# Kernel tuning notes

Measured on AMD Instinct MI355X. Metric: run time of the kernel, lower is better.

Reference implementation:

```python
import jax, jax.numpy as jnp
import numpy as np

BIG = 1e9  # finite stand-in for float('inf') so gradients stay clean
K_ITERS = 256  # Bellman-Ford relaxation sweeps (converges for paths up to K edges)
DIRS = [(-1, -1), (-1, 0), (-1, 1), (0, -1), (0, 1), (1, -1), (1, 0), (1, 1)]


def setup_inputs() -> dict:
    key = jax.random.key(0)
    ks = jax.random.split(key, 4)
    H, W, C = 256, 256, 128
    features = jax.random.normal(ks[0], (H, W, C), dtype=jnp.float32)
    return {
        "features": features,
        "delta": jnp.float32(0.1),
        "gamma": jnp.float32(1.0),
        "beta": jnp.float32(1.0),
        "w1": jax.random.normal(ks[1], (C, C // 4), dtype=jnp.float32) * 0.05,
        "b1": jnp.zeros((C // 4,), dtype=jnp.float32),
        "w2": jax.random.normal(ks[2], (C // 4, 1), dtype=jnp.float32) * 0.05,
        "b2": jnp.zeros((1,), dtype=jnp.float32),
        "start_node": jnp.zeros((2,), dtype=jnp.int32),
        "end_node": jnp.array([H - 1, W - 1], dtype=jnp.int32),
    }


def _avg_pool3(x):
    # x: (C, H, W); 3x3 avg pool, stride 1, pad 1, count_include_pad=True (torch default)
    s = jax.lax.reduce_window(x, 0.0, jax.lax.add, (1, 3, 3), (1, 1, 1),
                              ((0, 0), (1, 1), (1, 1)))
    return s / 9.0


def _heuristic_grid(features, delta, gamma, beta, w1, b1, w2, b2, end_node):
    H, W, C = features.shape
    all_feats = features.reshape(H * W, C)
    C_lf = C // 2
    feats_lf = all_feats[:, :C_lf]
    feats_hf = all_feats[:, C_lf:]

    # Sobel gradient magnitude per channel -> geodesic grid
    sobel_x = jnp.array([[-1, 0, 1], [-2, 0, 2], [-1, 0, 1]], dtype=features.dtype)
    sobel_y = jnp.array([[-1, -2, -1], [0, 0, 0], [1, 2, 1]], dtype=features.dtype)
    sobel = jnp.stack([sobel_x, sobel_y])[:, None]  # (2,1,3,3) OIHW
    x = jnp.transpose(features, (2, 0, 1))[:, None]  # (C,1,H,W)
    grad = jax.lax.conv_general_dilated(x, sobel, (1, 1), ((1, 1), (1, 1)),
                                        dimension_numbers=("NCHW", "OIHW", "NCHW"))
    grad_mag = jnp.sqrt(jnp.sum(grad * grad, axis=1))  # (C,H,W)
    geodesic_grid = jnp.mean(grad_mag, axis=0)  # (H,W)

    # Local variance of high-frequency channels
    hf = jnp.transpose(feats_hf.reshape(H, W, -1), (2, 0, 1))  # (C_hf,H,W)
    var_hf = jnp.sum(_avg_pool3(hf * hf) - _avg_pool3(hf) ** 2, axis=0)  # (H,W)
    info_goal_hf = var_hf[end_node[0], end_node[1]]
    scattering = info_goal_hf - var_hf

    # Absorption cost: distance of low-freq feats to goal low-freq feats
    end_feat_lf = feats_lf.reshape(H, W, -1)[end_node[0], end_node[1]]
    absorption = jnp.linalg.norm(feats_lf - end_feat_lf[None, :], axis=1).reshape(H, W)

    # Gating MLP
    h = jax.nn.relu(all_feats @ w1 + b1)
    omega = jax.nn.sigmoid(h @ w2 + b2).reshape(H, W)

    d, g, b = jax.nn.softplus(delta), jax.nn.softplus(gamma), jax.nn.softplus(beta)
    return jax.nn.relu(d * geodesic_grid + omega * g * scattering + (1 - omega) * b * absorption)


def _cost_grid(features):
    H, W, _ = features.shape
    fn = features / jnp.maximum(jnp.linalg.norm(features, axis=-1, keepdims=True), 1e-12)
    cost = jnp.full((H, W, 8), BIG, dtype=features.dtype)
    for i, (dx, dy) in enumerate(DIRS):
        sc_h = slice(max(0, -dx), H - max(0, dx))
        sc_w = slice(max(0, -dy), W - max(0, dy))
        sn_h = slice(max(0, dx), H + min(0, dx))
        sn_w = slice(max(0, dy), W + min(0, dy))
        sim = jnp.sum(fn[sc_h, sc_w] * fn[sn_h, sn_w], axis=-1)
        cost = cost.at[sc_h, sc_w, i].set(1.0 - sim)
    return cost


def _shift_big(a, dx, dy):
    H, W = a.shape
    p = jnp.pad(a, 1, constant_values=BIG)
    return jax.lax.dynamic_slice(p, (1 - dx, 1 - dy), (H, W))


def _distance_map(cost, start_node):
    # Parallel Bellman-Ford relaxation: equals the A* g_score map for shortest
    # paths with <= K_ITERS edges (nonnegative affinity costs).
    H, W, _ = cost.shape
    dist0 = jnp.full((H, W), BIG, dtype=cost.dtype).at[start_node[0], start_node[1]].set(0.0)

    def body(dist, _):
        d = dist
        for i, (dx, dy) in enumerate(DIRS):
            d = jnp.minimum(d, _shift_big(dist + cost[:, :, i], dx, dy))
        return d, None

    dist, _ = jax.lax.scan(body, dist0, None, length=K_ITERS)
    return jnp.minimum(dist, BIG)


def reference(features, delta, gamma, beta, w1, b1, w2, b2, start_node, end_node):
    heuristic = _heuristic_grid(features, delta, gamma, beta, w1, b1, w2, b2, end_node)
    cost = _cost_grid(features)
    dist = _distance_map(cost, start_node)
    # (H, W, 10): [heuristic | 8 directional edge costs | g_score distance map]
    return jnp.concatenate([heuristic[..., None], cost, dist[..., None]], axis=-1)
```

## Files before the change

### kernel.cpp

```cpp
#include <hip/hip_runtime.h>
#include <math.h>

#define Hd 256
#define Wd 256
#define Cd 128
#define BIGV 1.0e9f

static __device__ __forceinline__ float softplus_f(float x) {
    return fmaxf(x, 0.0f) + log1pf(expf(-fabsf(x)));
}

#define FMAXBITS 0x7F7FFFFF
template<int CTRL, int RM>
static __device__ __forceinline__ float dpp_mv(float x) {
    return __int_as_float(__builtin_amdgcn_update_dpp(
        FMAXBITS, __float_as_int(x), CTRL, RM, 0xF, false));
}
template<int CTRL, int RM>
static __device__ __forceinline__ float dpp_min(float x) {
    return fminf(x, dpp_mv<CTRL, RM>(x));
}
static __device__ __forceinline__ float wave_prefmin(float x) {
    x = dpp_min<0x111, 0xF>(x);
    x = dpp_min<0x112, 0xF>(x);
    x = dpp_min<0x114, 0xF>(x);
    x = dpp_min<0x118, 0xF>(x);
    x = dpp_min<0x142, 0xA>(x);
    x = dpp_min<0x143, 0xC>(x);
    return x;
}

#define TILE 16
#define HPX 18
#define PXN 324
#define SP  325
#define CHUNK 32

__global__ __launch_bounds__(256) void k_cost(
    const float* __restrict__ feat,
    float* __restrict__ out, float* __restrict__ costP)
{
    __shared__ float stage[CHUNK * SP];
    __shared__ float normL[PXN];

    const int t  = threadIdx.x;
    const int r0 = blockIdx.y * TILE;
    const int c0 = blockIdx.x * TILE;

    const int lr = t >> 4, lc = t & 15;
    const int r = r0 + lr, c = c0 + lc;
    const int px0 = (lr + 1) * HPX + (lc + 1);

    float dotv[8];
#pragma unroll
    for (int j = 0; j < 8; ++j) dotv[j] = 0.0f;

    for (int ch0 = 0; ch0 < Cd; ch0 += CHUNK) {
        __syncthreads();
        for (int i = t; i < PXN * 8; i += 256) {
            int px = i >> 3, f4 = i & 7;
            int pr = px / HPX;
            int pc = px - pr * HPX;
            int gr = r0 - 1 + pr, gc = c0 - 1 + pc;
            float4 v = make_float4(0.f, 0.f, 0.f, 0.f);
            if ((unsigned)gr < Hd && (unsigned)gc < Wd) {
                v = *reinterpret_cast<const float4*>(
                        &feat[(((gr << 8) + gc) * Cd) + ch0 + (f4 << 2)]);
            }
            int chb = f4 << 2;
            stage[(chb + 0) * SP + px] = v.x;
            stage[(chb + 1) * SP + px] = v.y;
            stage[(chb + 2) * SP + px] = v.z;
            stage[(chb + 3) * SP + px] = v.w;
        }
        __syncthreads();
        for (int px = t; px < PXN; px += 256) {
            float s = 0.0f;
#pragma unroll
            for (int ch = 0; ch < CHUNK; ++ch) {
                float v = stage[ch * SP + px];
                s = fmaf(v, v, s);
            }
            if (ch0 == 0) normL[px] = s; else normL[px] += s;
        }
        for (int ch = 0; ch < CHUNK; ++ch) {
            const float* pl = stage + ch * SP + px0;
            float x  = pl[0];
            float n0 = pl[-HPX - 1], n1 = pl[-HPX], n2 = pl[-HPX + 1];
            float n3 = pl[-1],                      n4 = pl[1];
            float n5 = pl[HPX - 1],  n6 = pl[HPX],  n7 = pl[HPX + 1];

            dotv[0] = fmaf(x, n0, dotv[0]);
            dotv[1] = fmaf(x, n1, dotv[1]);
            dotv[2] = fmaf(x, n2, dotv[2]);
            dotv[3] = fmaf(x, n3, dotv[3]);
            dotv[4] = fmaf(x, n4, dotv[4]);
            dotv[5] = fmaf(x, n5, dotv[5]);
            dotv[6] = fmaf(x, n6, dotv[6]);
            dotv[7] = fmaf(x, n7, dotv[7]);
        }
    }
    __syncthreads();

    const int p = (r << 8) + c;
    float np = fmaxf(sqrtf(normL[px0]), 1e-12f);
    const int drr[8] = {-1,-1,-1, 0, 0, 1, 1, 1};
    const int dcc[8] = {-1, 0, 1,-1, 1,-1, 0, 1};
    const int nof[8] = {-HPX-1,-HPX,-HPX+1,-1,1,HPX-1,HPX,HPX+1};
#pragma unroll
    for (int j = 0; j < 8; ++j) {
        int nr = r + drr[j], nc = c + dcc[j];
        float cj;
        if ((unsigned)nr < Hd && (unsigned)nc < Wd) {
            float nn = fmaxf(sqrtf(normL[px0 + nof[j]]), 1e-12f);
            cj = 1.0f - dotv[j] / (np * nn);
        } else {
            cj = BIGV;
        }
        costP[(j << 16) + p] = cj;
        out[p * 10 + 1 + j]  = cj;
    }
}

__global__ __launch_bounds__(64) void k_scan(
    const float* __restrict__ costP, float* __restrict__ PR, float* __restrict__ PRm)
{
    const int r = blockIdx.x;
    const int l = threadIdx.x;
    const int base = (r << 8) + (l << 2);

    {
        const float4 c4 = *(const float4*)&costP[(4 << 16) + base];
        float a0 = c4.x, a1 = a0 + c4.y, a2 = a1 + c4.z, a3 = a2 + c4.w;
        float ta = a3;
#pragma unroll
        for (int o = 1; o < 64; o <<= 1) {
            float xa = __shfl_up(ta, o, 64);
            if (l >= o) ta += xa;
        }
        float ea = __shfl_up(ta, 1, 64); if (l == 0) ea = 0.0f;
        float4 P; P.x = ea; P.y = ea + a0; P.z = ea + a1; P.w = ea + a2;
        *(float4*)&PR[base] = P;
    }
    {
        const float4 m = *(const float4*)&costP[(3 << 16) + (r << 8) + (252 - (l << 2))];
        float w0 = m.w, w1_ = m.z, w2_ = m.y, w3 = m.x;
        float a0 = w0, a1 = a0 + w1_, a2 = a1 + w2_, a3 = a2 + w3;
        float ta = a3;
#pragma unroll
        for (int o = 1; o < 64; o <<= 1) {
            float xa = __shfl_up(ta, o, 64);
            if (l >= o) ta += xa;
        }
        float ea = __shfl_up(ta, 1, 64); if (l == 0) ea = 0.0f;
        float4 P; P.x = ea; P.y = ea + a0; P.z = ea + a1; P.w = ea + a2;
        *(float4*)&PRm[base] = P;
    }
}

#define PIPE 8

static __device__ __forceinline__ float4 ld4m(const float* p, int r, int l, int M) {
    if (!M) return *(const float4*)&p[(r << 8) + (l << 2)];
    float4 v = *(const float4*)&p[(r << 8) + (252 - (l << 2))];
    return make_float4(v.w, v.z, v.y, v.x);
}

__global__ __launch_bounds__(256) void k_main(
    const float* __restrict__ feat,
    const float* __restrict__ w1, const float* __restrict__ b1,
    const float* __restrict__ w2, const float* __restrict__ b2,
    const float* __restrict__ dlt, const float* __restrict__ gmm,
    const float* __restrict__ bta, const int* __restrict__ endn,
    const float* __restrict__ costP, const float* __restrict__ PR,
    const float* __restrict__ PRm, const int* __restrict__ startn,
    float* __restrict__ out, float* __restrict__ distQ)
{
    if (blockIdx.x < 4) {
        const int l = threadIdx.x;
        if (l >= 64) return;
        const int sw = blockIdx.x;
        const int M     = sw & 1;
        const int vdown = (sw < 2);
        const int sr = startn[0];
        const int sc = M ? (255 - startn[1]) : startn[1];
        const float* __restrict__ PRu = M ? PRm : PR;
        const int pInc = vdown ? (M ? 5 : 7) : (M ? 0 : 2);
        const int pStr = vdown ? 6 : 1;
        const int pDec = vdown ? (M ? 7 : 5) : (M ? 2 : 0);
        const float* __restrict__ cInP = costP + (pInc << 16);
        const float* __restrict__ cStP = costP + (pStr << 16);
        const float* __restrict__ cDeP = costP + (pDec << 16);
        float* __restrict__ O = distQ + (sw << 16);
        const int iStart = vdown ? sr : (255 - sr);

        const float4 BIG4 = make_float4(BIGV, BIGV, BIGV, BIGV);

        float4 sv = BIG4;
        {
            int kk = sc - (l << 2);
            if (kk == 0) sv.x = 0.0f;
            if (kk == 1) sv.y = 0.0f;
            if (kk == 2) sv.z = 0.0f;
            if (kk == 3) sv.w = 0.0f;
        }

#define ROW_OF(ii)  (vdown ? ((ii) > 255 ? 255 : (ii)) : (255 - ((ii) > 255 ? 255 : (ii))))
#define ROWP_OF(ii) (vdown ? (((ii) - 1) < 0 ? 0 : (((ii) - 1) > 255 ? 255 : ((ii) - 1))) \
                           : (255 - (((ii) - 1) < 0 ? 0 : (((ii) - 1) > 255 ? 255 : ((ii) - 1)))))

        float4 bPR[PIPE], bI[PIPE], bS[PIPE], bD[PIPE];
#pragma unroll
        for (int k = 0; k < PIPE; ++k) {
            int rP = ROW_OF(k), rC = ROWP_OF(k);
            bPR[k] = *(const float4*)&PRu[(rP << 8) + (l << 2)];
            bI[k]  = ld4m(cInP, rC, l, M);
            bS[k]  = ld4m(cStP, rC, l, M);
            bD[k]  = ld4m(cDeP, rC, l, M);
        }

        float4 Dp = BIG4;
        for (int ib = 0; ib < 256; ib += PIPE) {
#pragma unroll
            for (int k = 0; k < PIPE; ++k) {
                const int i = ib + k;
                const int r = vdown ? i : 255 - i;
                float4 PR_c = bPR[k], cI_c = bI[k], cS_c = bS[k], cD_c = bD[k];

                float tS0 = Dp.x + cS_c.x, tS1 = Dp.y + cS_c.y,
                      tS2 = Dp.z + cS_c.z, tS3 = Dp.w + cS_c.w;
                float tI0 = Dp.x + cI_c.x, tI1 = Dp.y + cI_c.y,
                      tI2 = Dp.z + cI_c.z, tI3 = Dp.w + cI_c.w;
                float tD0 = Dp.x + cD_c.x, tD1 = Dp.y + cD_c.y,
                      tD2 = Dp.z + cD_c.z, tD3 = Dp.w + cD_c.w;
                float tIm = dpp_mv<0x138, 0xF>(tI3);
                float tDn = dpp_mv<0x130, 0xF>(tD0);
                float4 cand;
                cand.x = fminf(tS0, fminf(tIm, tD1));
                cand.y = fminf(tS1, fminf(tI0, tD2));
                cand.z = fminf(tS2, fminf(tI1, tD3));
                cand.w = fminf(tS3, fminf(tI2, tDn));
                if (i == iStart) {
                    cand.x = fminf(cand.x, sv.x);
                    cand.y = fminf(cand.y, sv.y);
                    cand.z = fminf(cand.z, sv.z);
                    cand.w = fminf(cand.w, sv.w);
                }
                float z0 = cand.x - PR_c.x;
                float z1 = fminf(cand.y - PR_c.y, z0);
                float z2 = fminf(cand.z - PR_c.z, z1);
                float z3 = fminf(cand.w - PR_c.w, z2);
                float w  = wave_prefmin(z3);
                float e  = dpp_mv<0x138, 0xF>(w);
                float4 D;
                D.x = PR_c.x + fminf(z0, e);
                D.y = PR_c.y + fminf(z1, e);
                D.z = PR_c.z + fminf(z2, e);
                D.w = PR_c.w + fminf(z3, e);

                *(float4*)&O[(r << 8) + (l << 2)] = D;
                Dp = D;

                {
                    const int jn = i + PIPE;
                    int rP = ROW_OF(jn), rC = ROWP_OF(jn);
                    bPR[k] = *(const float4*)&PRu[(rP << 8) + (l << 2)];
                    bI[k]  = ld4m(cInP, rC, l, M);
                    bS[k]  = ld4m(cStP, rC, l, M);
                    bD[k]  = ld4m(cDeP, rC, l, M);
                }
            }
        }
#undef ROW_OF
#undef ROWP_OF
        return;
    }

    __shared__ float  stage[CHUNK * SP];
    __shared__ float4 w1L[Cd * 8];
    __shared__ float  endfL[64];
    __shared__ float  vendL[64];
    __shared__ float  vendS;

    const int t  = threadIdx.x;
    const int b  = blockIdx.x - 4;
    const int r0 = (b >> 4) * TILE;
    const int c0 = (b & 15) * TILE;

    for (int i = t; i < Cd * 8; i += 256) w1L[i] = ((const float4*)w1)[i];
    const int er = endn[0], ec = endn[1];
    if (t < 64) {
        endfL[t] = feat[(er * Wd + ec) * Cd + t];
        float s1 = 0.0f, s2 = 0.0f;
#pragma unroll
        for (int dr = -1; dr <= 1; ++dr)
#pragma unroll
            for (int dc = -1; dc <= 1; ++dc) {
                int gr = er + dr, gc = ec + dc;
                if ((unsigned)gr < Hd && (unsigned)gc < Wd) {
                    float x = feat[((gr << 8) + gc) * Cd + 64 + t];
                    s1 += x; s2 = fmaf(x, x, s2);
                }
            }
        float m = s1 * (1.0f / 9.0f);
        vendL[t] = s2 * (1.0f / 9.0f) - m * m;
    }

    const int lr = t >> 4, lc = t & 15;
    const int r = r0 + lr, c = c0 + lc;
    const int px0 = (lr + 1) * HPX + (lc + 1);

    float4 hv[8];
#pragma unroll
    for (int j = 0; j < 8; ++j) hv[j] = make_float4(0.f, 0.f, 0.f, 0.f);
    float gm_acc = 0.0f, var_acc = 0.0f, abs_acc = 0.0f;

    for (int ch0 = 0; ch0 < Cd; ch0 += CHUNK) {
        __syncthreads();
        for (int i = t; i < PXN * 8; i += 256) {
            int px = i >> 3, f4 = i & 7;
            int pr = px / HPX;
            int pc = px - pr * HPX;
            int gr = r0 - 1 + pr, gc = c0 - 1 + pc;
            float4 v = make_float4(0.f, 0.f, 0.f, 0.f);
            if ((unsigned)gr < Hd && (unsigned)gc < Wd) {
                v = *reinterpret_cast<const float4*>(
                        &feat[(((gr << 8) + gc) * Cd) + ch0 + (f4 << 2)]);
            }
            int chb = f4 << 2;
            stage[(chb + 0) * SP + px] = v.x;
            stage[(chb + 1) * SP + px] = v.y;
            stage[(chb + 2) * SP + px] = v.z;
            stage[(chb + 3) * SP + px] = v.w;
        }
        __syncthreads();
        const bool is_hf = (ch0 >= 64);
        for (int ch = 0; ch < CHUNK; ++ch) {
            const float* pl = stage + ch * SP + px0;
            float x  = pl[0];
            float n0 = pl[-HPX - 1], n1 = pl[-HPX], n2 = pl[-HPX + 1];
            float n3 = pl[-1],                      n4 = pl[1];
            float n5 = pl[HPX - 1],  n6 = pl[HPX],  n7 = pl[HPX + 1];

            float gx = (n2 + 2.f * n4 + n7) - (n0 + 2.f * n3 + n5);
            float gy = (n5 + 2.f * n6 + n7) - (n0 + 2.f * n1 + n2);
            gm_acc += sqrtf(gx * gx + gy * gy);

            if (is_hf) {
                float s1 = x + n0 + n1 + n2 + n3 + n4 + n5 + n6 + n7;
                float s2 = x*x + n0*n0 + n1*n1 + n2*n2 + n3*n3 + n4*n4
                         + n5*n5 + n6*n6 + n7*n7;
                float m = s1 * (1.0f / 9.0f);
                var_acc += s2 * (1.0f / 9.0f) - m * m;
            } else {
                float dlf = x - endfL[ch0 + ch];
                abs_acc = fmaf(dlf, dlf, abs_acc);
            }

            const float4* __restrict__ wr4 = &w1L[(ch0 + ch) << 3];
#pragma unroll
            for (int j4 = 0; j4 < 8; ++j4) {
                float4 wv = wr4[j4];
                hv[j4].x = fmaf(x, wv.x, hv[j4].x);
                hv[j4].y = fmaf(x, wv.y, hv[j4].y);
                hv[j4].z = fmaf(x, wv.z, hv[j4].z);
                hv[j4].w = fmaf(x, wv.w, hv[j4].w);
            }
        }
    }
    __syncthreads();

    if (t < 64) {
        float v = vendL[t];
#pragma unroll
        for (int o = 32; o > 0; o >>= 1) v += __shfl_down(v, o, 64);
        if (t == 0) vendS = v;
    }
    __syncthreads();
    const float vend = vendS;

    const int p = (r << 8) + c;
    float geo  = gm_acc * (1.0f / 128.0f);
    float absp = sqrtf(abs_acc);
    float o = b2[0];
#pragma unroll
    for (int j4 = 0; j4 < 8; ++j4) {
#pragma unroll
        for (int cc = 0; cc < 4; ++cc) {
            int j = (j4 << 2) + cc;
            float hj = fmaxf(((const float*)&hv[j4])[cc] + b1[j], 0.0f);
            o = fmaf(hj, w2[j], o);
        }
    }
    float omg = 1.0f / (1.0f + expf(-o));
    float dS = softplus_f(dlt[0]);
    float gS = softplus_f(gmm[0]);
    float bS = softplus_f(bta[0]);
    float heur = dS * geo + omg * gS * (vend - var_acc)
               + (1.0f - omg) * bS * absp;
    out[p * 10] = fmaxf(heur, 0.0f);
}

__global__ __launch_bounds__(256) void k_merge(
    const float* __restrict__ distQ, float* __restrict__ out)
{
    int p  = blockIdx.x * 256 + threadIdx.x;
    int pm = (p & ~255) + (255 - (p & 255));
    float v = fminf(fminf(distQ[p],           distQ[(2 << 16) + p]),
                    fminf(distQ[(1 << 16) + pm], distQ[(3 << 16) + pm]));
    out[p * 10 + 9] = fminf(v, BIGV);
}

extern "C" void kernel_launch(void* const* d_in, const int* in_sizes, int n_in,
                              void* d_out, int out_size, void* d_ws, size_t ws_size,
                              hipStream_t stream)
{
    const float* feat  = (const float*)d_in[0];
    const float* dlt   = (const float*)d_in[1];
    const float* gmm   = (const float*)d_in[2];
    const float* bta   = (const float*)d_in[3];
    const float* w1    = (const float*)d_in[4];
    const float* b1    = (const float*)d_in[5];
    const float* w2    = (const float*)d_in[6];
    const float* b2    = (const float*)d_in[7];
    const int*   startn= (const int*)d_in[8];
    const int*   endn  = (const int*)d_in[9];
    float* out = (float*)d_out;
    float* ws  = (float*)d_ws;

    float* costP = ws;
    float* PR    = ws + 8  * 65536;
    float* PRm   = ws + 9  * 65536;
    float* distQ = ws + 10 * 65536;

    dim3 g16(16, 16);
    k_cost<<<g16, 256, 0, stream>>>(feat, out, costP);
    k_scan<<<256, 64, 0, stream>>>(costP, PR, PRm);
    k_main<<<260, 256, 0, stream>>>(feat, w1, b1, w2, b2, dlt, gmm, bta, endn,
                                    costP, PR, PRm, startn, out, distQ);
    k_merge<<<256, 256, 0, stream>>>(distQ, out);
}
```

Baseline: 198.3 us.

## Interleave two directional sweeps per wavefront and raise sweep wave priority

Each sweep wavefront now runs two sweeps (the normal and the column-mirrored variant) interleaved in one loop instead of one sweep per block. The two dependency chains are independent, so their DPP scans and loads can overlap and hide each other's latency, and the launch needs two fewer blocks. The sweep waves also raise their scheduling priority with s_setprio. Prefetch depth drops from 8 to 4 rows to keep register use in check, which could expose more memory latency, and the row-serial critical path is now shared by two chains in one wave.

```diff
diff --git a/kernel.cpp b/kernel.cpp
--- a/kernel.cpp
+++ b/kernel.cpp
@@ -158,7 +158,7 @@
     }
 }
 
-#define PIPE 8
+#define PIPE 4
 
 static __device__ __forceinline__ float4 ld4m(const float* p, int r, int l, int M) {
     if (!M) return *(const float4*)&p[(r << 8) + (l << 2)];
@@ -176,98 +176,146 @@
     const float* __restrict__ PRm, const int* __restrict__ startn,
     float* __restrict__ out, float* __restrict__ distQ)
 {
-    if (blockIdx.x < 4) {
+    if (blockIdx.x < 2) {
         const int l = threadIdx.x;
         if (l >= 64) return;
-        const int sw = blockIdx.x;
-        const int M     = sw & 1;
-        const int vdown = (sw < 2);
-        const int sr = startn[0];
-        const int sc = M ? (255 - startn[1]) : startn[1];
-        const float* __restrict__ PRu = M ? PRm : PR;
-        const int pInc = vdown ? (M ? 5 : 7) : (M ? 0 : 2);
-        const int pStr = vdown ? 6 : 1;
-        const int pDec = vdown ? (M ? 7 : 5) : (M ? 2 : 0);
-        const float* __restrict__ cInP = costP + (pInc << 16);
-        const float* __restrict__ cStP = costP + (pStr << 16);
-        const float* __restrict__ cDeP = costP + (pDec << 16);
-        float* __restrict__ O = distQ + (sw << 16);
+        __builtin_amdgcn_s_setprio(1);
+        const int pair  = blockIdx.x;
+        const int vdown = (pair == 0);
+        const int sr  = startn[0];
+        const int scA = startn[1];
+        const int scB = 255 - startn[1];
+        const float* __restrict__ PRa = PR;
+        const float* __restrict__ PRb = PRm;
+        const int pIncA = vdown ? 7 : 2, pDecA = vdown ? 5 : 0;
+        const int pIncB = vdown ? 5 : 0, pDecB = vdown ? 7 : 2;
+        const int pStr  = vdown ? 6 : 1;
+        const float* __restrict__ cInA = costP + (pIncA << 16);
+        const float* __restrict__ cStA = costP + (pStr  << 16);
+        const float* __restrict__ cDeA = costP + (pDecA << 16);
+        const float* __restrict__ cInB = costP + (pIncB << 16);
+        const float* __restrict__ cStB = cStA;
+        const float* __restrict__ cDeB = costP + (pDecB << 16);
+        float* __restrict__ OA = distQ + ((pair ? 2 : 0) << 16);
+        float* __restrict__ OB = distQ + ((pair ? 3 : 1) << 16);
         const int iStart = vdown ? sr : (255 - sr);
 
         const float4 BIG4 = make_float4(BIGV, BIGV, BIGV, BIGV);
 
-        float4 sv = BIG4;
+        float4 svA = BIG4, svB = BIG4;
         {
-            int kk = sc - (l << 2);
-            if (kk == 0) sv.x = 0.0f;
-            if (kk == 1) sv.y = 0.0f;
-            if (kk == 2) sv.z = 0.0f;
-            if (kk == 3) sv.w = 0.0f;
+            int ka = scA - (l << 2);
+            if (ka == 0) svA.x = 0.0f;
+            if (ka == 1) svA.y = 0.0f;
+            if (ka == 2) svA.z = 0.0f;
+            if (ka == 3) svA.w = 0.0f;
+            int kb = scB - (l << 2);
+            if (kb == 0) svB.x = 0.0f;
+            if (kb == 1) svB.y = 0.0f;
+            if (kb == 2) svB.z = 0.0f;
+            if (kb == 3) svB.w = 0.0f;
         }
 
 #define ROW_OF(ii)  (vdown ? ((ii) > 255 ? 255 : (ii)) : (255 - ((ii) > 255 ? 255 : (ii))))
 #define ROWP_OF(ii) (vdown ? (((ii) - 1) < 0 ? 0 : (((ii) - 1) > 255 ? 255 : ((ii) - 1))) \
                            : (255 - (((ii) - 1) < 0 ? 0 : (((ii) - 1) > 255 ? 255 : ((ii) - 1)))))
 
+        float4 aPR[PIPE], aI[PIPE], aS[PIPE], aD[PIPE];
         float4 bPR[PIPE], bI[PIPE], bS[PIPE], bD[PIPE];
 #pragma unroll
         for (int k = 0; k < PIPE; ++k) {
             int rP = ROW_OF(k), rC = ROWP_OF(k);
-            bPR[k] = *(const float4*)&PRu[(rP << 8) + (l << 2)];
-            bI[k]  = ld4m(cInP, rC, l, M);
-            bS[k]  = ld4m(cStP, rC, l, M);
-            bD[k]  = ld4m(cDeP, rC, l, M);
-        }
-
-        float4 Dp = BIG4;
+            aPR[k] = *(const float4*)&PRa[(rP << 8) + (l << 2)];
+            aI[k]  = ld4m(cInA, rC, l, 0);
+            aS[k]  = ld4m(cStA, rC, l, 0);
+            aD[k]  = ld4m(cDeA, rC, l, 0);
+            bPR[k] = *(const float4*)&PRb[(rP << 8) + (l << 2)];
+            bI[k]  = ld4m(cInB, rC, l, 1);
+            bS[k]  = ld4m(cStB, rC, l, 1);
+            bD[k]  = ld4m(cDeB, rC, l, 1);
+        }
+
+        float4 DpA = BIG4, DpB = BIG4;
         for (int ib = 0; ib < 256; ib += PIPE) {
 #pragma unroll
             for (int k = 0; k < PIPE; ++k) {
                 const int i = ib + k;
                 const int r = vdown ? i : 255 - i;
-                float4 PR_c = bPR[k], cI_c = bI[k], cS_c = bS[k], cD_c = bD[k];
-
-                float tS0 = Dp.x + cS_c.x, tS1 = Dp.y + cS_c.y,
-                      tS2 = Dp.z + cS_c.z, tS3 = Dp.w + cS_c.w;
-                float tI0 = Dp.x + cI_c.x, tI1 = Dp.y + cI_c.y,
-                      tI2 = Dp.z + cI_c.z, tI3 = Dp.w + cI_c.w;
-                float tD0 = Dp.x + cD_c.x, tD1 = Dp.y + cD_c.y,
-                      tD2 = Dp.z + cD_c.z, tD3 = Dp.w + cD_c.w;
-                float tIm = dpp_mv<0x138, 0xF>(tI3);
-                float tDn = dpp_mv<0x130, 0xF>(tD0);
-                float4 cand;
-                cand.x = fminf(tS0, fminf(tIm, tD1));
-                cand.y = fminf(tS1, fminf(tI0, tD2));
-                cand.z = fminf(tS2, fminf(tI1, tD3));
-                cand.w = fminf(tS3, fminf(tI2, tDn));
+
+                float4 PA = aPR[k], AI = aI[k], AS = aS[k], AD = aD[k];
+                float aS0 = DpA.x + AS.x, aS1 = DpA.y + AS.y,
+                      aS2 = DpA.z + AS.z, aS3 = DpA.w + AS.w;
+                float aI0 = DpA.x + AI.x, aI1 = DpA.y + AI.y,
+                      aI2 = DpA.z + AI.z, aI3 = DpA.w + AI.w;
+                float aD0 = DpA.x + AD.x, aD1 = DpA.y + AD.y,
+                      aD2 = DpA.z + AD.z, aD3 = DpA.w + AD.w;
+                float aIm = dpp_mv<0x138, 0xF>(aI3);
+                float aDn = dpp_mv<0x130, 0xF>(aD0);
+                float4 cA;
+                cA.x = fminf(aS0, fminf(aIm, aD1));
+                cA.y = fminf(aS1, fminf(aI0, aD2));
+                cA.z = fminf(aS2, fminf(aI1, aD3));
+                cA.w = fminf(aS3, fminf(aI2, aDn));
+
+                float4 PB = bPR[k], BI = bI[k], BS = bS[k], BD = bD[k];
+                float bS0 = DpB.x + BS.x, bS1 = DpB.y + BS.y,
+                      bS2 = DpB.z + BS.z, bS3 = DpB.w + BS.w;
+                float bI0 = DpB.x + BI.x, bI1 = DpB.y + BI.y,
+                      bI2 = DpB.z + BI.z, bI3 = DpB.w + BI.w;
+                float bD0 = DpB.x + BD.x, bD1 = DpB.y + BD.y,
+                      bD2 = DpB.z + BD.z, bD3 = DpB.w + BD.w;
+                float bIm = dpp_mv<0x138, 0xF>(bI3);
+                float bDn = dpp_mv<0x130, 0xF>(bD0);
+                float4 cB;
+                cB.x = fminf(bS0, fminf(bIm, bD1));
+                cB.y = fminf(bS1, fminf(bI0, bD2));
+                cB.z = fminf(bS2, fminf(bI1, bD3));
+                cB.w = fminf(bS3, fminf(bI2, bDn));
+
                 if (i == iStart) {
-                    cand.x = fminf(cand.x, sv.x);
-                    cand.y = fminf(cand.y, sv.y);
-                    cand.z = fminf(cand.z, sv.z);
-                    cand.w = fminf(cand.w, sv.w);
+                    cA.x = fminf(cA.x, svA.x); cA.y = fminf(cA.y, svA.y);
+                    cA.z = fminf(cA.z, svA.z); cA.w = fminf(cA.w, svA.w);
+                    cB.x = fminf(cB.x, svB.x); cB.y = fminf(cB.y, svB.y);
+                    cB.z = fminf(cB.z, svB.z); cB.w = fminf(cB.w, svB.w);
                 }
-                float z0 = cand.x - PR_c.x;
-                float z1 = fminf(cand.y - PR_c.y, z0);
-                float z2 = fminf(cand.z - PR_c.z, z1);
-                float z3 = fminf(cand.w - PR_c.w, z2);
-                float w  = wave_prefmin(z3);
-                float e  = dpp_mv<0x138, 0xF>(w);
-                float4 D;
-                D.x = PR_c.x + fminf(z0, e);
-                D.y = PR_c.y + fminf(z1, e);
-                D.z = PR_c.z + fminf(z2, e);
-                D.w = PR_c.w + fminf(z3, e);
-
-                *(float4*)&O[(r << 8) + (l << 2)] = D;
-                Dp = D;
+
+                float za0 = cA.x - PA.x;
+                float za1 = fminf(cA.y - PA.y, za0);
+                float za2 = fminf(cA.z - PA.z, za1);
+                float za3 = fminf(cA.w - PA.w, za2);
+                float zb0 = cB.x - PB.x;
+                float zb1 = fminf(cB.y - PB.y, zb0);
+                float zb2 = fminf(cB.z - PB.z, zb1);
+                float zb3 = fminf(cB.w - PB.w, zb2);
+                float wa  = wave_prefmin(za3);
+                float wb  = wave_prefmin(zb3);
+                float ea  = dpp_mv<0x138, 0xF>(wa);
+                float eb  = dpp_mv<0x138, 0xF>(wb);
+                float4 DA, DB;
+                DA.x = PA.x + fminf(za0, ea);
+                DA.y = PA.y + fminf(za1, ea);
+                DA.z = PA.z + fminf(za2, ea);
+                DA.w = PA.w + fminf(za3, ea);
+                DB.x = PB.x + fminf(zb0, eb);
+                DB.y = PB.y + fminf(zb1, eb);
+                DB.z = PB.z + fminf(zb2, eb);
+                DB.w = PB.w + fminf(zb3, eb);
+
+                *(float4*)&OA[(r << 8) + (l << 2)] = DA;
+                *(float4*)&OB[(r << 8) + (l << 2)] = DB;
+                DpA = DA; DpB = DB;
 
                 {
                     const int jn = i + PIPE;
                     int rP = ROW_OF(jn), rC = ROWP_OF(jn);
-                    bPR[k] = *(const float4*)&PRu[(rP << 8) + (l << 2)];
-                    bI[k]  = ld4m(cInP, rC, l, M);
-                    bS[k]  = ld4m(cStP, rC, l, M);
-                    bD[k]  = ld4m(cDeP, rC, l, M);
+                    aPR[k] = *(const float4*)&PRa[(rP << 8) + (l << 2)];
+                    aI[k]  = ld4m(cInA, rC, l, 0);
+                    aS[k]  = ld4m(cStA, rC, l, 0);
+                    aD[k]  = ld4m(cDeA, rC, l, 0);
+                    bPR[k] = *(const float4*)&PRb[(rP << 8) + (l << 2)];
+                    bI[k]  = ld4m(cInB, rC, l, 1);
+                    bS[k]  = ld4m(cStB, rC, l, 1);
+                    bD[k]  = ld4m(cDeB, rC, l, 1);
                 }
             }
         }
@@ -283,7 +331,7 @@
     __shared__ float  vendS;
 
     const int t  = threadIdx.x;
-    const int b  = blockIdx.x - 4;
+    const int b  = blockIdx.x - 2;
     const int r0 = (b >> 4) * TILE;
     const int c0 = (b & 15) * TILE;
 
@@ -436,7 +484,7 @@
     dim3 g16(16, 16);
     k_cost<<<g16, 256, 0, stream>>>(feat, out, costP);
     k_scan<<<256, 64, 0, stream>>>(costP, PR, PRm);
-    k_main<<<260, 256, 0, stream>>>(feat, w1, b1, w2, b2, dlt, gmm, bta, endn,
+    k_main<<<258, 256, 0, stream>>>(feat, w1, b1, w2, b2, dlt, gmm, bta, endn,
                                     costP, PR, PRm, startn, out, distQ);
     k_merge<<<256, 256, 0, stream>>>(distQ, out);
 }
```

Measured after the change: 209.1 us. +5.5%, slower.
